# Performance work log

Measured on AMD Instinct MI355X. Metric: run time of the kernel, lower is better.

## Reference

```python
import jax, jax.numpy as jnp
import numpy as np

D_MODEL = 1024
HEADS = 16
D_KEY = D_MODEL // HEADS


def setup_inputs() -> dict:
    key = jax.random.key(0)
    ks = jax.random.split(key, 7)
    B, S = 4, 2048
    queries = jax.random.normal(ks[0], (B, S, D_MODEL), dtype=jnp.float32)
    keys = jax.random.normal(ks[1], (B, S, D_MODEL), dtype=jnp.float32)
    values = jax.random.normal(ks[2], (B, S, D_MODEL), dtype=jnp.float32)
    scale = 1.0 / np.sqrt(D_MODEL)
    # Per-head projection weights, torch Linear layout [out=d_key, in=d_model], stacked over heads
    Wq = jax.random.uniform(ks[3], (HEADS, D_KEY, D_MODEL), jnp.float32, -scale, scale)
    Wk = jax.random.uniform(ks[4], (HEADS, D_KEY, D_MODEL), jnp.float32, -scale, scale)
    Wv = jax.random.uniform(ks[5], (HEADS, D_KEY, D_MODEL), jnp.float32, -scale, scale)
    Wo = jax.random.uniform(ks[6], (D_MODEL, D_MODEL), jnp.float32, -scale, scale)
    return {"queries": queries, "keys": keys, "values": values,
            "Wq": Wq, "Wk": Wk, "Wv": Wv, "Wo": Wo}


def reference(queries, keys, values, Wq, Wk, Wv, Wo):
    # Project per head: [B,S,D] x [H,K,D] -> [B,H,S,K]
    q = jnp.einsum('bsd,hkd->bhsk', queries, Wq)
    k = jnp.einsum('bsd,hkd->bhsk', keys, Wk)
    v = jnp.einsum('bsd,hkd->bhsk', values, Wv)
    attn = jnp.einsum('bhqk,bhsk->bhqs', q, k) / jnp.sqrt(jnp.float32(D_KEY))
    attn = jax.nn.softmax(attn, axis=-1)
    out = jnp.einsum('bhqs,bhsk->bhqk', attn, v)  # [B,H,S,K]
    B, H, S, K = out.shape
    # concat heads along last dim (head order = torch cat order)
    out = out.transpose(0, 2, 1, 3).reshape(B, S, H * K)
    return out @ Wo.T
```

## Files before the change

### kernel.cpp

```cpp
#include <hip/hip_runtime.h>
#include <hip/hip_bf16.h>

typedef __attribute__((ext_vector_type(8))) short short8;
typedef __attribute__((ext_vector_type(4))) short short4v;
typedef __attribute__((ext_vector_type(4))) float f32x4;
typedef __bf16 bf16x8 __attribute__((ext_vector_type(8)));

#define DEVI static __device__ __forceinline__

DEVI short f2bs(float f) {
    union { __hip_bfloat16 h; short s; } u;
    u.h = __float2bfloat16(f);
    return u.s;
}

DEVI f32x4 mfma16(short8 a, short8 b, f32x4 c) {
    return __builtin_amdgcn_mfma_f32_16x16x32_bf16(
        __builtin_bit_cast(bf16x8, a), __builtin_bit_cast(bf16x8, b), c, 0, 0, 0);
}

DEVI void glds16(const short* g, short* l) {
    __builtin_amdgcn_global_load_lds((const __attribute__((address_space(1))) void*)g,
                                     (__attribute__((address_space(3))) void*)l, 16, 0, 0);
}

__global__ __launch_bounds__(256) void cvt3(const float4* __restrict__ a,
                                            const float4* __restrict__ b,
                                            const float4* __restrict__ c,
                                            short4v* __restrict__ da,
                                            short4v* __restrict__ db,
                                            short4v* __restrict__ dc, int n4) {
    int i = blockIdx.x * 256 + threadIdx.x;
    if (i < n4) {
        float4 v;
        short4v s;
        v = a[i]; s.x = f2bs(v.x); s.y = f2bs(v.y); s.z = f2bs(v.z); s.w = f2bs(v.w); da[i] = s;
        v = b[i]; s.x = f2bs(v.x); s.y = f2bs(v.y); s.z = f2bs(v.z); s.w = f2bs(v.w); db[i] = s;
        v = c[i]; s.x = f2bs(v.x); s.y = f2bs(v.y); s.z = f2bs(v.z); s.w = f2bs(v.w); dc[i] = s;
    }
}

__global__ __launch_bounds__(256) void cvt4(const float4* __restrict__ a,
                                            const float4* __restrict__ b,
                                            const float4* __restrict__ c,
                                            const float4* __restrict__ d,
                                            short4v* __restrict__ da,
                                            short4v* __restrict__ db,
                                            short4v* __restrict__ dc,
                                            short4v* __restrict__ dd, int n4) {
    int i = blockIdx.x * 256 + threadIdx.x;
    if (i < n4) {
        float4 v;
        short4v s;
        v = a[i]; s.x = f2bs(v.x); s.y = f2bs(v.y); s.z = f2bs(v.z); s.w = f2bs(v.w); da[i] = s;
        v = b[i]; s.x = f2bs(v.x); s.y = f2bs(v.y); s.z = f2bs(v.z); s.w = f2bs(v.w); db[i] = s;
        v = c[i]; s.x = f2bs(v.x); s.y = f2bs(v.y); s.z = f2bs(v.z); s.w = f2bs(v.w); dc[i] = s;
        v = d[i]; s.x = f2bs(v.x); s.y = f2bs(v.y); s.z = f2bs(v.z); s.w = f2bs(v.w); dd[i] = s;
    }
}

template <typename EpiT>
DEVI void gemm_body(const short* A, const short* Bw, short* smem, int m0, int n0, EpiT epi) {
    short* As = smem;
    short* Bs = smem + 8192;
    const int t = threadIdx.x;
    const int lane = t & 63, w = t >> 6;
    const int col = lane & 15, quad = lane >> 4;
    const int wm = (w & 1) * 64, wn = (w >> 1) * 64;

    f32x4 acc[4][4];
#pragma unroll
    for (int i = 0; i < 4; ++i)
#pragma unroll
        for (int j = 0; j < 4; ++j) acc[i][j] = (f32x4){0.f, 0.f, 0.f, 0.f};

    for (int kt = 0; kt < 16; ++kt) {
        const int k0 = kt * 64;
#pragma unroll
        for (int j = 0; j < 4; ++j) {
            int cbase = (j * 4 + w) * 64;
            int c = cbase + lane;
            int row = c >> 3, kc = (c & 7) ^ (row & 7);
            glds16(A + (size_t)(m0 + row) * 1024 + k0 + kc * 8, As + cbase * 8);
        }
#pragma unroll
        for (int j = 0; j < 4; ++j) {
            int cbase = (j * 4 + w) * 64;
            int c = cbase + lane;
            int row = c >> 3, kc = (c & 7) ^ (row & 7);
            glds16(Bw + (size_t)(n0 + row) * 1024 + k0 + kc * 8, Bs + cbase * 8);
        }
        __syncthreads();
#pragma unroll
        for (int ks = 0; ks < 2; ++ks) {
            short8 a[4], b[4];
#pragma unroll
            for (int i = 0; i < 4; ++i) {
                int row = wm + i * 16 + col;
                int kc = (ks * 4 + quad) ^ (col & 7);
                a[i] = *(const short8*)(As + (row * 8 + kc) * 8);
            }
#pragma unroll
            for (int i = 0; i < 4; ++i) {
                int row = wn + i * 16 + col;
                int kc = (ks * 4 + quad) ^ (col & 7);
                b[i] = *(const short8*)(Bs + (row * 8 + kc) * 8);
            }
#pragma unroll
            for (int mi = 0; mi < 4; ++mi)
#pragma unroll
                for (int ni = 0; ni < 4; ++ni)
                    acc[mi][ni] = mfma16(a[mi], b[ni], acc[mi][ni]);
        }
        __syncthreads();
    }
    epi(acc, wm, wn, col, quad);
}

__global__ __launch_bounds__(256) void qkv_gemm(const short* __restrict__ xq,
                                                const short* __restrict__ xk,
                                                const short* __restrict__ xv,
                                                const short* __restrict__ wq,
                                                const short* __restrict__ wk,
                                                const short* __restrict__ wv,
                                                short* __restrict__ qp,
                                                short* __restrict__ kp,
                                                short* __restrict__ vpt, float qscale) {
    __shared__ __align__(16) short smem[16896];
    const int z = blockIdx.z;
    const int m0 = blockIdx.y * 128, n0 = blockIdx.x * 128;
    const short* A = (z == 0) ? xq : (z == 1) ? xk : xv;
    const short* W = (z == 0) ? wq : (z == 1) ? wk : wv;

    if (z < 2) {
        short* outs = (z == 0) ? qp : kp;
        const float scale = (z == 0) ? qscale : 1.0f;
        gemm_body(A, W, smem, m0, n0, [&](f32x4 (&acc)[4][4], int wm, int wn, int col, int quad) {
#pragma unroll
            for (int mi = 0; mi < 4; ++mi)
#pragma unroll
                for (int ni = 0; ni < 4; ++ni)
#pragma unroll
                    for (int r = 0; r < 4; ++r) {
                        int m = m0 + wm + mi * 16 + quad * 4 + r;
                        int n = n0 + wn + ni * 16 + col;
                        size_t off =
                            ((size_t)((m >> 11) * 16 + (n >> 6)) * 2048 + (m & 2047)) * 64 +
                            (n & 63);
                        outs[off] = f2bs(acc[mi][ni][r] * scale);
                    }
        });
    } else {
        gemm_body(A, W, smem, m0, n0, [&](f32x4 (&acc)[4][4], int wm, int wn, int col, int quad) {
            short* T = smem;
#pragma unroll
            for (int mi = 0; mi < 4; ++mi)
#pragma unroll
                for (int ni = 0; ni < 4; ++ni) {
                    int n_l = wn + ni * 16 + col;
                    int m_l = wm + mi * 16 + quad * 4;
                    short4v sv;
                    sv.x = f2bs(acc[mi][ni][0]); sv.y = f2bs(acc[mi][ni][1]);
                    sv.z = f2bs(acc[mi][ni][2]); sv.w = f2bs(acc[mi][ni][3]);
                    *(short4v*)(T + n_l * 132 + m_l) = sv;
                }
            __syncthreads();
            int t = threadIdx.x;
            int nrow = t >> 1, mh = (t & 1) * 64;
            int b = m0 >> 11, s0 = m0 & 2047;
            size_t base = ((size_t)(b * 1024 + n0 + nrow)) * 2048 + s0 + mh;
#pragma unroll
            for (int j = 0; j < 16; ++j) {
                unsigned long long vv = *(const unsigned long long*)(T + nrow * 132 + mh + j * 4);
                *(unsigned long long*)(vpt + base + j * 4) = vv;
            }
        });
    }
}

__global__ __launch_bounds__(256) void out_gemm(const short* __restrict__ ao,
                                                const short* __restrict__ wo,
                                                float* __restrict__ outf) {
    __shared__ __align__(16) short smem[16896];
    const int m0 = blockIdx.y * 128, n0 = blockIdx.x * 128;
    gemm_body(ao, wo, smem, m0, n0, [&](f32x4 (&acc)[4][4], int wm, int wn, int col, int quad) {
#pragma unroll
        for (int mi = 0; mi < 4; ++mi)
#pragma unroll
            for (int ni = 0; ni < 4; ++ni)
#pragma unroll
                for (int r = 0; r < 4; ++r) {
                    int m = m0 + wm + mi * 16 + quad * 4 + r;
                    int n = n0 + wn + ni * 16 + col;
                    outf[(size_t)m * 1024 + n] = acc[mi][ni][r];
                }
    });
}

__global__ __launch_bounds__(256, 4) void flash_attn(const short* __restrict__ qp,
                                                     const short* __restrict__ kp,
                                                     const short* __restrict__ vpt,
                                                     short* __restrict__ ao) {
    __shared__ __align__(16) short smem[8192 + 8192 + 4 * 1152];
    short* Ks = smem;
    short* Vs = smem + 8192;

    const int t = threadIdx.x, lane = t & 63, w = t >> 6;
    const int col = lane & 15, quad = lane >> 4;
    const int bh = blockIdx.x, q0 = blockIdx.y * 128;
    const short* qb = qp + (size_t)bh * 2048 * 64;
    const short* kb = kp + (size_t)bh * 2048 * 64;
    const short* vb = vpt + (size_t)bh * 64 * 2048;
    short* Pw = smem + 16384 + w * 1152;

#pragma unroll
    for (int j = 0; j < 4; ++j) {
        int cbase = (j * 4 + w) * 64;
        int c = cbase + lane;
        int row = c >> 3, kc = (c & 7) ^ (row & 7);
        glds16(qb + (size_t)(q0 + row) * 64 + kc * 8, Ks + cbase * 8);
    }
    __syncthreads();
    short8 bQ[2][2];
#pragma unroll
    for (int qi = 0; qi < 2; ++qi)
#pragma unroll
        for (int ks = 0; ks < 2; ++ks) {
            int row = w * 32 + qi * 16 + col;
            int kc = (ks * 4 + quad) ^ (col & 7);
            bQ[qi][ks] = *(const short8*)(Ks + (row * 8 + kc) * 8);
        }
    __syncthreads();

    f32x4 acc_o[2][4];
    float l_r[2] = {0.f, 0.f};
#pragma unroll
    for (int qi = 0; qi < 2; ++qi)
#pragma unroll
        for (int ni = 0; ni < 4; ++ni) acc_o[qi][ni] = (f32x4){0.f, 0.f, 0.f, 0.f};

    const int vdk = w * 16 + (lane >> 4) + 0;
    (void)vdk;

    for (int kt = 0; kt < 16; ++kt) {
#pragma unroll
        for (int j = 0; j < 4; ++j) {
            int cbase = (j * 4 + w) * 64;
            int c = cbase + lane;
            int row = c >> 3, kc = (c & 7) ^ (row & 7);
            glds16(kb + (size_t)(kt * 128 + row) * 64 + kc * 8, Ks + cbase * 8);
        }
#pragma unroll
        for (int j = 0; j < 4; ++j) {
            int m = w * 4 + j;
            int dk = m * 4 + (lane >> 4);
            int sc = (lane & 15) ^ (dk & 15);
            glds16(vb + (size_t)dk * 2048 + kt * 128 + sc * 8, Vs + m * 512);
        }
        __syncthreads();

#pragma unroll
        for (int g = 0; g < 4; ++g) {
#pragma unroll
            for (int h = 0; h < 2; ++h) {
                int kei = g * 2 + h;
                f32x4 st[2];
                st[0] = (f32x4){0.f, 0.f, 0.f, 0.f};
                st[1] = (f32x4){0.f, 0.f, 0.f, 0.f};
#pragma unroll
                for (int ks = 0; ks < 2; ++ks) {
                    int row = kei * 16 + col;
                    int kc = (ks * 4 + quad) ^ (col & 7);
                    short8 aK = *(const short8*)(Ks + (row * 8 + kc) * 8);
#pragma unroll
                    for (int qi = 0; qi < 2; ++qi) st[qi] = mfma16(aK, bQ[qi][ks], st[qi]);
                }
#pragma unroll
                for (int qi = 0; qi < 2; ++qi) {
                    float p0 = __builtin_amdgcn_exp2f(st[qi][0]);
                    float p1 = __builtin_amdgcn_exp2f(st[qi][1]);
                    float p2 = __builtin_amdgcn_exp2f(st[qi][2]);
                    float p3 = __builtin_amdgcn_exp2f(st[qi][3]);
                    l_r[qi] += (p0 + p1) + (p2 + p3);
                    short4v pv;
                    pv.x = f2bs(p0); pv.y = f2bs(p1); pv.z = f2bs(p2); pv.w = f2bs(p3);
                    *(short4v*)(Pw + (qi * 16 + col) * 36 + h * 16 + quad * 4) = pv;
                }
            }
            short8 pa[2];
#pragma unroll
            for (int qi = 0; qi < 2; ++qi)
                pa[qi] = *(const short8*)(Pw + (qi * 16 + col) * 36 + quad * 8);
#pragma unroll
            for (int ni = 0; ni < 4; ++ni) {
                int dk = ni * 16 + col;
                short8 bv = *(const short8*)(Vs + dk * 128 + (((g * 4 + quad) ^ col) * 8));
#pragma unroll
                for (int qi = 0; qi < 2; ++qi)
                    acc_o[qi][ni] = mfma16(pa[qi], bv, acc_o[qi][ni]);
            }
        }
        __syncthreads();
    }

#pragma unroll
    for (int qi = 0; qi < 2; ++qi) {
        l_r[qi] += __shfl_xor(l_r[qi], 16);
        l_r[qi] += __shfl_xor(l_r[qi], 32);
    }
    const int b = bh >> 4, hd = bh & 15;
#pragma unroll
    for (int qi = 0; qi < 2; ++qi)
#pragma unroll
        for (int r = 0; r < 4; ++r) {
            float lq = __shfl(l_r[qi], quad * 4 + r);
            float inv = 1.0f / lq;
            int q = q0 + w * 32 + qi * 16 + quad * 4 + r;
#pragma unroll
            for (int ni = 0; ni < 4; ++ni)
                ao[((size_t)(b * 2048 + q)) * 1024 + hd * 64 + ni * 16 + col] =
                    f2bs(acc_o[qi][ni][r] * inv);
        }
}

extern "C" void kernel_launch(void* const* d_in, const int* in_sizes, int n_in,
                              void* d_out, int out_size, void* d_ws, size_t ws_size,
                              hipStream_t stream) {
    const float* q  = (const float*)d_in[0];
    const float* k  = (const float*)d_in[1];
    const float* v  = (const float*)d_in[2];
    const float* Wq = (const float*)d_in[3];
    const float* Wk = (const float*)d_in[4];
    const float* Wv = (const float*)d_in[5];
    const float* Wo = (const float*)d_in[6];
    float* out = (float*)d_out;

    short* ws = (short*)d_ws;
    const size_t SZ = (size_t)64 * 2048 * 64;
    const size_t WZ = (size_t)1024 * 1024;
    short* xq  = ws;
    short* xk  = ws + SZ;
    short* xv  = ws + 2 * SZ;
    short* qp  = ws + 3 * SZ;
    short* kp  = ws + 4 * SZ;
    short* wqb = ws + 5 * SZ;
    short* wkb = wqb + WZ;
    short* wvb = wqb + 2 * WZ;
    short* wob = wqb + 3 * WZ;
    short* ao  = xq;
    short* vpt = xk;

    const float QSCALE = 0.125f * 1.44269504088896f;

    cvt3<<<dim3(8192), dim3(256), 0, stream>>>((const float4*)q, (const float4*)k,
                                               (const float4*)v, (short4v*)xq, (short4v*)xk,
                                               (short4v*)xv, (int)(SZ / 4));
    cvt4<<<dim3(1024), dim3(256), 0, stream>>>((const float4*)Wq, (const float4*)Wk,
                                               (const float4*)Wv, (const float4*)Wo,
                                               (short4v*)wqb, (short4v*)wkb, (short4v*)wvb,
                                               (short4v*)wob, (int)(WZ / 4));
    dim3 blk(256);
    qkv_gemm<<<dim3(8, 64, 3), blk, 0, stream>>>(xq, xk, xv, wqb, wkb, wvb, qp, kp, vpt, QSCALE);
    flash_attn<<<dim3(64, 16), blk, 0, stream>>>(qp, kp, vpt, ao);
    out_gemm<<<dim3(8, 64), blk, 0, stream>>>(ao, wob, out);
}
```

Baseline: 397.8 us.

## Merge conversion kernels, stage Q/K epilogue through LDS, swizzle P tile

The two fp32-to-bf16 conversion kernels are merged into one launch so a launch and its tail are removed. The Q/K projection epilogue now writes the tile to LDS first and then stores 16-byte vectors to global memory, replacing scattered 2-byte stores. The per-wave P buffer in flash attention drops its padded stride of 36 for a stride of 32 with an XOR swizzle, which shrinks LDS use and aims to avoid bank conflicts. Costs are an extra barrier and slightly more LDS in the GEMM epilogue.

```diff
diff --git a/kernel.cpp b/kernel.cpp
--- a/kernel.cpp
+++ b/kernel.cpp
@@ -24,38 +24,34 @@
                                      (__attribute__((address_space(3))) void*)l, 16, 0, 0);
 }
 
-__global__ __launch_bounds__(256) void cvt3(const float4* __restrict__ a,
-                                            const float4* __restrict__ b,
-                                            const float4* __restrict__ c,
-                                            short4v* __restrict__ da,
-                                            short4v* __restrict__ db,
-                                            short4v* __restrict__ dc, int n4) {
-    int i = blockIdx.x * 256 + threadIdx.x;
-    if (i < n4) {
-        float4 v;
-        short4v s;
-        v = a[i]; s.x = f2bs(v.x); s.y = f2bs(v.y); s.z = f2bs(v.z); s.w = f2bs(v.w); da[i] = s;
-        v = b[i]; s.x = f2bs(v.x); s.y = f2bs(v.y); s.z = f2bs(v.z); s.w = f2bs(v.w); db[i] = s;
-        v = c[i]; s.x = f2bs(v.x); s.y = f2bs(v.y); s.z = f2bs(v.z); s.w = f2bs(v.w); dc[i] = s;
-    }
-}
-
-__global__ __launch_bounds__(256) void cvt4(const float4* __restrict__ a,
-                                            const float4* __restrict__ b,
-                                            const float4* __restrict__ c,
-                                            const float4* __restrict__ d,
-                                            short4v* __restrict__ da,
-                                            short4v* __restrict__ db,
-                                            short4v* __restrict__ dc,
-                                            short4v* __restrict__ dd, int n4) {
-    int i = blockIdx.x * 256 + threadIdx.x;
-    if (i < n4) {
-        float4 v;
-        short4v s;
-        v = a[i]; s.x = f2bs(v.x); s.y = f2bs(v.y); s.z = f2bs(v.z); s.w = f2bs(v.w); da[i] = s;
-        v = b[i]; s.x = f2bs(v.x); s.y = f2bs(v.y); s.z = f2bs(v.z); s.w = f2bs(v.w); db[i] = s;
-        v = c[i]; s.x = f2bs(v.x); s.y = f2bs(v.y); s.z = f2bs(v.z); s.w = f2bs(v.w); dc[i] = s;
-        v = d[i]; s.x = f2bs(v.x); s.y = f2bs(v.y); s.z = f2bs(v.z); s.w = f2bs(v.w); dd[i] = s;
+__global__ __launch_bounds__(256) void cvt_all(const float4* __restrict__ q,
+                                               const float4* __restrict__ k,
+                                               const float4* __restrict__ v,
+                                               const float4* __restrict__ wq,
+                                               const float4* __restrict__ wk,
+                                               const float4* __restrict__ wv,
+                                               const float4* __restrict__ wo,
+                                               short4v* __restrict__ dq,
+                                               short4v* __restrict__ dk,
+                                               short4v* __restrict__ dv,
+                                               short4v* __restrict__ dwq,
+                                               short4v* __restrict__ dwk,
+                                               short4v* __restrict__ dwv,
+                                               short4v* __restrict__ dwo) {
+    int bid = blockIdx.x;
+    float4 x;
+    short4v s;
+    if (bid < 8192) {
+        int i = bid * 256 + threadIdx.x;
+        x = q[i]; s.x = f2bs(x.x); s.y = f2bs(x.y); s.z = f2bs(x.z); s.w = f2bs(x.w); dq[i] = s;
+        x = k[i]; s.x = f2bs(x.x); s.y = f2bs(x.y); s.z = f2bs(x.z); s.w = f2bs(x.w); dk[i] = s;
+        x = v[i]; s.x = f2bs(x.x); s.y = f2bs(x.y); s.z = f2bs(x.z); s.w = f2bs(x.w); dv[i] = s;
+    } else {
+        int i = (bid - 8192) * 256 + threadIdx.x;
+        x = wq[i]; s.x = f2bs(x.x); s.y = f2bs(x.y); s.z = f2bs(x.z); s.w = f2bs(x.w); dwq[i] = s;
+        x = wk[i]; s.x = f2bs(x.x); s.y = f2bs(x.y); s.z = f2bs(x.z); s.w = f2bs(x.w); dwk[i] = s;
+        x = wv[i]; s.x = f2bs(x.x); s.y = f2bs(x.y); s.z = f2bs(x.z); s.w = f2bs(x.w); dwv[i] = s;
+        x = wo[i]; s.x = f2bs(x.x); s.y = f2bs(x.y); s.z = f2bs(x.z); s.w = f2bs(x.w); dwo[i] = s;
     }
 }
 
@@ -126,7 +122,7 @@
                                                 short* __restrict__ qp,
                                                 short* __restrict__ kp,
                                                 short* __restrict__ vpt, float qscale) {
-    __shared__ __align__(16) short smem[16896];
+    __shared__ __align__(16) short smem[17408];
     const int z = blockIdx.z;
     const int m0 = blockIdx.y * 128, n0 = blockIdx.x * 128;
     const short* A = (z == 0) ? xq : (z == 1) ? xk : xv;
@@ -136,19 +132,27 @@
         short* outs = (z == 0) ? qp : kp;
         const float scale = (z == 0) ? qscale : 1.0f;
         gemm_body(A, W, smem, m0, n0, [&](f32x4 (&acc)[4][4], int wm, int wn, int col, int quad) {
+            short* T = smem;
 #pragma unroll
             for (int mi = 0; mi < 4; ++mi)
 #pragma unroll
                 for (int ni = 0; ni < 4; ++ni)
 #pragma unroll
-                    for (int r = 0; r < 4; ++r) {
-                        int m = m0 + wm + mi * 16 + quad * 4 + r;
-                        int n = n0 + wn + ni * 16 + col;
-                        size_t off =
-                            ((size_t)((m >> 11) * 16 + (n >> 6)) * 2048 + (m & 2047)) * 64 +
-                            (n & 63);
-                        outs[off] = f2bs(acc[mi][ni][r] * scale);
-                    }
+                    for (int r = 0; r < 4; ++r)
+                        T[(wm + mi * 16 + quad * 4 + r) * 136 + wn + ni * 16 + col] =
+                            f2bs(acc[mi][ni][r] * scale);
+            __syncthreads();
+            int t = threadIdx.x;
+            int ml = t >> 1, nh = (t & 1) * 64;
+            int m = m0 + ml;
+            int b = m >> 11, s = m & 2047;
+#pragma unroll
+            for (int j = 0; j < 8; ++j) {
+                int n = n0 + nh + j * 8;
+                short8 vv = *(const short8*)(T + ml * 136 + nh + j * 8);
+                size_t off = ((size_t)(b * 16 + (n >> 6)) * 2048 + s) * 64 + (n & 63);
+                *(short8*)(outs + off) = vv;
+            }
         });
     } else {
         gemm_body(A, W, smem, m0, n0, [&](f32x4 (&acc)[4][4], int wm, int wn, int col, int quad) {
@@ -201,7 +205,7 @@
                                                      const short* __restrict__ kp,
                                                      const short* __restrict__ vpt,
                                                      short* __restrict__ ao) {
-    __shared__ __align__(16) short smem[8192 + 8192 + 4 * 1152];
+    __shared__ __align__(16) short smem[8192 + 8192 + 4096];
     short* Ks = smem;
     short* Vs = smem + 8192;
 
@@ -211,7 +215,7 @@
     const short* qb = qp + (size_t)bh * 2048 * 64;
     const short* kb = kp + (size_t)bh * 2048 * 64;
     const short* vb = vpt + (size_t)bh * 64 * 2048;
-    short* Pw = smem + 16384 + w * 1152;
+    short* Pw = smem + 16384 + w * 1024;
 
 #pragma unroll
     for (int j = 0; j < 4; ++j) {
@@ -238,9 +242,6 @@
     for (int qi = 0; qi < 2; ++qi)
 #pragma unroll
         for (int ni = 0; ni < 4; ++ni) acc_o[qi][ni] = (f32x4){0.f, 0.f, 0.f, 0.f};
-
-    const int vdk = w * 16 + (lane >> 4) + 0;
-    (void)vdk;
 
     for (int kt = 0; kt < 16; ++kt) {
 #pragma unroll
@@ -284,13 +285,17 @@
                     l_r[qi] += (p0 + p1) + (p2 + p3);
                     short4v pv;
                     pv.x = f2bs(p0); pv.y = f2bs(p1); pv.z = f2bs(p2); pv.w = f2bs(p3);
-                    *(short4v*)(Pw + (qi * 16 + col) * 36 + h * 16 + quad * 4) = pv;
+                    int row = qi * 16 + col;
+                    int ch = (h * 2 + (quad >> 1)) ^ (row & 3);
+                    *(short4v*)(Pw + row * 32 + ch * 8 + (quad & 1) * 4) = pv;
                 }
             }
             short8 pa[2];
 #pragma unroll
-            for (int qi = 0; qi < 2; ++qi)
-                pa[qi] = *(const short8*)(Pw + (qi * 16 + col) * 36 + quad * 8);
+            for (int qi = 0; qi < 2; ++qi) {
+                int row = qi * 16 + col;
+                pa[qi] = *(const short8*)(Pw + row * 32 + (quad ^ (row & 3)) * 8);
+            }
 #pragma unroll
             for (int ni = 0; ni < 4; ++ni) {
                 int dk = ni * 16 + col;
@@ -352,13 +357,10 @@
 
     const float QSCALE = 0.125f * 1.44269504088896f;
 
-    cvt3<<<dim3(8192), dim3(256), 0, stream>>>((const float4*)q, (const float4*)k,
-                                               (const float4*)v, (short4v*)xq, (short4v*)xk,
-                                               (short4v*)xv, (int)(SZ / 4));
-    cvt4<<<dim3(1024), dim3(256), 0, stream>>>((const float4*)Wq, (const float4*)Wk,
-                                               (const float4*)Wv, (const float4*)Wo,
-                                               (short4v*)wqb, (short4v*)wkb, (short4v*)wvb,
-                                               (short4v*)wob, (int)(WZ / 4));
+    cvt_all<<<dim3(9216), dim3(256), 0, stream>>>(
+        (const float4*)q, (const float4*)k, (const float4*)v, (const float4*)Wq,
+        (const float4*)Wk, (const float4*)Wv, (const float4*)Wo, (short4v*)xq, (short4v*)xk,
+        (short4v*)xv, (short4v*)wqb, (short4v*)wkb, (short4v*)wvb, (short4v*)wob);
     dim3 blk(256);
     qkv_gemm<<<dim3(8, 64, 3), blk, 0, stream>>>(xq, xk, xv, wqb, wkb, wvb, qp, kp, vpt, QSCALE);
     flash_attn<<<dim3(64, 16), blk, 0, stream>>>(qp, kp, vpt, ao);
```

Result: faster. 346.3 us (-13.0%).
